# Kernel optimization log

Hardware: AMD Instinct MI355X
Metric: run time of the kernel (lower is better)

## Reference

```python
import jax, jax.numpy as jnp
import numpy as np
from functools import partial

K = 64
KERNEL_SIZE = 16
TAU = 10.0
THETA = 0.5
GAMMA = 10.0
ALPHA = float(np.exp(-1.0 / TAU))
BETA = 1.0 - ALPHA

@jax.custom_vjp
def spike(x):
    return (x >= 0).astype(x.dtype)

def _spike_fwd(x):
    return spike(x), x

def _spike_bwd(x, g):
    surrogate = GAMMA * jnp.maximum(1.0 - GAMMA * jnp.abs(x), 0.0)
    return (g * surrogate,)

spike.defvjp(_spike_fwd, _spike_bwd)

def setup_inputs() -> dict:
    key = jax.random.key(0)
    k1, k2 = jax.random.split(key)
    B, T = 256, 4096
    x = jax.random.normal(k1, (B, 1, T), dtype=jnp.float32)
    # conv weight [K, 1, ks], init N(0, 1/sqrt(ks))
    W = jax.random.normal(k2, (K, 1, KERNEL_SIZE), dtype=jnp.float32) / np.sqrt(KERNEL_SIZE)
    return {"x": x, "W": W}

def _forward(x, W):
    B = x.shape[0]
    x = x.reshape(B, 1, -1)  # [B,1,T]
    # causal conv: left pad ks-1 -> output length T
    u = jax.lax.conv_general_dilated(
        x, W,
        window_strides=(1,),
        padding=[(KERNEL_SIZE - 1, 0)],
        dimension_numbers=("NCH", "OIH", "NCH"),
    )  # [B,K,T]
    u_t = jnp.transpose(u, (2, 0, 1))  # [T,B,K]
    v0 = jnp.zeros((B, K), dtype=x.dtype)

    def step(v, ut):
        v = ALPHA * v + BETA * ut                      # leak + input
        s_raw = spike(v - THETA)                        # [B,K]
        winner = jax.lax.stop_gradient(jnp.argmax(v, axis=1))  # [B]
        winner_spiked = jnp.take_along_axis(s_raw, winner[:, None], axis=1)  # [B,1]
        wta_mask = jax.nn.one_hot(winner, K, dtype=s_raw.dtype) * winner_spiked
        s = s_raw * wta_mask
        v = v - s * THETA                               # reset
        return v, s

    _, spikes_t = jax.lax.scan(step, v0, u_t)  # [T,B,K]
    return jnp.transpose(spikes_t, (1, 2, 0))  # [B,K,T]

def reference(x, W):
    return _forward(x, W)
```

## Files before the change

kernel.cpp:

```cpp
#include <hip/hip_runtime.h>

#define T_LEN  4096
#define KS     16
#define NSEG   8
#define SEG_CH 32
#define WARM_CH 20
#define USTRIDE 18

#define ALPHA_F 0.9048374180359595f
#define BETA_F  0.09516258196404048f
#define THETA_F 0.5f

__device__ __forceinline__ float wave64_max_all(float v) {
  float m, t;
  asm("s_nop 1\n\t"
      "v_max_f32 %0, %2, %2 quad_perm:[1,0,3,2] row_mask:0xf bank_mask:0xf\n\t"
      "s_nop 1\n\t"
      "v_max_f32 %0, %0, %0 quad_perm:[2,3,0,1] row_mask:0xf bank_mask:0xf\n\t"
      "s_nop 1\n\t"
      "v_max_f32 %0, %0, %0 row_half_mirror row_mask:0xf bank_mask:0xf\n\t"
      "s_nop 1\n\t"
      "v_max_f32 %0, %0, %0 row_mirror row_mask:0xf bank_mask:0xf\n\t"
      "v_mov_b32 %1, %0\n\t"
      "s_nop 1\n\t"
      "v_permlane32_swap_b32 %1, %0\n\t"
      "s_nop 1\n\t"
      "v_max_f32 %0, %0, %1\n\t"
      "v_mov_b32 %1, %0\n\t"
      "s_nop 1\n\t"
      "v_permlane16_swap_b32 %1, %0\n\t"
      "s_nop 1\n\t"
      "v_max_f32 %0, %0, %1"
      : "=&v"(m), "=&v"(t)
      : "v"(v));
  return m;
}

__global__ __launch_bounds__(128, 4)
void convlif_wta_kernel(const float* __restrict__ x, const float* __restrict__ W,
                        float* __restrict__ out) {
  const int blk  = blockIdx.x;
  const int b    = blk >> 3;
  const int seg  = blk & (NSEG - 1);
  const int wave = threadIdx.x >> 6;
  const int lane = threadIdx.x & 63;

  const int cout0  = seg * SEG_CH;
  const int cstart = (cout0 > WARM_CH) ? (cout0 - WARM_CH) : 0;
  const int cend   = cout0 + SEG_CH;
  const int wpairs = (cout0 - cstart) >> 1;
  const int npair  = (cend - cstart) >> 1;

  __shared__ float dbuf[2][2][64][USTRIDE];

  const float4* xv4 = reinterpret_cast<const float4*>(x + (size_t)b * T_LEN);
  float* orow = out + ((size_t)(b * 64 + lane)) * T_LEN;

  if (wave == 1) {
    float w[KS];
    {
      const float4* w4 = reinterpret_cast<const float4*>(W + lane * KS);
      #pragma unroll
      for (int q = 0; q < 4; ++q) {
        float4 a = w4[q];
        w[4*q+0] = a.x; w[4*q+1] = a.y; w[4*q+2] = a.z; w[4*q+3] = a.w;
      }
    }

    for (int p = 0; p < npair; ++p) {
      #pragma unroll
      for (int ch = 0; ch < 2; ++ch) {
        const int c = cstart + 2 * p + ch;
        float xf[32];
        if (c == 0) {
          #pragma unroll
          for (int m = 0; m < 16; ++m) xf[m] = 0.0f;
        } else {
          const int b4 = 4 * c - 4;
          #pragma unroll
          for (int q = 0; q < 4; ++q) {
            float4 a = xv4[b4 + q];
            xf[4*q+0] = a.x; xf[4*q+1] = a.y; xf[4*q+2] = a.z; xf[4*q+3] = a.w;
          }
        }
        #pragma unroll
        for (int q = 0; q < 4; ++q) {
          float4 a = xv4[4*c + q];
          xf[16+4*q+0] = a.x; xf[16+4*q+1] = a.y;
          xf[16+4*q+2] = a.z; xf[16+4*q+3] = a.w;
        }

        float* ur = &dbuf[p & 1][ch][lane][0];
        #pragma unroll
        for (int i = 0; i < 16; i += 2) {
          float acc0 = w[0] * xf[1 + i];
          #pragma unroll
          for (int j = 1; j < KS; ++j) acc0 = fmaf(w[j], xf[1 + i + j], acc0);
          float acc1 = w[0] * xf[2 + i];
          #pragma unroll
          for (int j = 1; j < KS; ++j) acc1 = fmaf(w[j], xf[2 + i + j], acc1);
          *reinterpret_cast<float2*>(ur + i) =
              make_float2(BETA_F * acc0, BETA_F * acc1);
        }
      }
      __syncthreads();
    }
    __syncthreads();
  } else {
    float v = 0.0f;

    __syncthreads();

    for (int q = 0; q < wpairs; ++q) {
      const int slot = q & 1;
      #pragma unroll
      for (int ch = 0; ch < 2; ++ch) {
        float u[16];
        {
          const float* ur = &dbuf[slot][ch][lane][0];
          #pragma unroll
          for (int i = 0; i < 16; i += 2) {
            float2 t2 = *reinterpret_cast<const float2*>(ur + i);
            u[i] = t2.x; u[i + 1] = t2.y;
          }
        }
        #pragma unroll
        for (int i = 0; i < 16; ++i) {
          float vr = fmaf(ALPHA_F, v, u[i]);
          float vm = vr - THETA_F;
          unsigned long long sp = __ballot(vr >= THETA_F);
          bool c1 = (vr >= THETA_F);
          v = c1 ? vm : vr;
          if (__builtin_expect((sp & (sp - 1ull)) != 0ull, 0)) {
            float m = wave64_max_all(vr);
            unsigned long long eq = __ballot(vr == m);
            bool win = (lane == __builtin_ctzll(eq));
            v = win ? vm : vr;
          }
        }
      }
      __syncthreads();
    }

    for (int q = wpairs; q < npair; ++q) {
      const int slot = q & 1;
      #pragma unroll
      for (int ch = 0; ch < 2; ++ch) {
        const int c = cstart + 2 * q + ch;
        float u[16];
        {
          const float* ur = &dbuf[slot][ch][lane][0];
          #pragma unroll
          for (int i = 0; i < 16; i += 2) {
            float2 t2 = *reinterpret_cast<const float2*>(ur + i);
            u[i] = t2.x; u[i + 1] = t2.y;
          }
        }
        float sv[16];
        #pragma unroll
        for (int i = 0; i < 16; ++i) {
          float vr = fmaf(ALPHA_F, v, u[i]);
          float vm = vr - THETA_F;
          unsigned long long sp = __ballot(vr >= THETA_F);
          bool c1 = (vr >= THETA_F);
          sv[i] = c1 ? 1.0f : 0.0f;
          v     = c1 ? vm : vr;
          if (__builtin_expect((sp & (sp - 1ull)) != 0ull, 0)) {
            float m = wave64_max_all(vr);
            unsigned long long eq = __ballot(vr == m);
            bool win = (lane == __builtin_ctzll(eq));
            sv[i] = win ? 1.0f : 0.0f;
            v     = win ? vm : vr;
          }
        }
        float4* pp = reinterpret_cast<float4*>(orow + (size_t)c * 16);
        pp[0] = make_float4(sv[0],  sv[1],  sv[2],  sv[3]);
        pp[1] = make_float4(sv[4],  sv[5],  sv[6],  sv[7]);
        pp[2] = make_float4(sv[8],  sv[9],  sv[10], sv[11]);
        pp[3] = make_float4(sv[12], sv[13], sv[14], sv[15]);
      }
      __syncthreads();
    }
  }
}

extern "C" void kernel_launch(void* const* d_in, const int* in_sizes, int n_in,
                              void* d_out, int out_size, void* d_ws, size_t ws_size,
                              hipStream_t stream) {
  const float* x   = (const float*)d_in[0];
  const float* W   = (const float*)d_in[1];
  float*       out = (float*)d_out;
  convlif_wta_kernel<<<dim3(256 * NSEG), dim3(128), 0, stream>>>(x, W, out);
}
```

Baseline: 106.1 us.

## Use three conv producer waves and halve time segments per batch row

Time is now split into 4 segments of 64 chunks instead of 8 segments of 32. Each block gets three producer waves that compute the convolution for three chunks per barrier interval into a triple-wide double buffer, feeding one scan wave. Fewer segments cut the duplicated warm-up scan work. The extra producer waves are meant to stop the single conv wave from limiting the serial scan. The trade-off is a longer serial scan per block and half as many blocks, which lowers parallelism across the GPU.

Result: slower. 148.6 us (+40.1%).

```diff
diff --git a/kernel.cpp b/kernel.cpp
--- a/kernel.cpp
+++ b/kernel.cpp
@@ -2,8 +2,8 @@
 
 #define T_LEN  4096
 #define KS     16
-#define NSEG   8
-#define SEG_CH 32
+#define NSEG   4
+#define SEG_CH 64
 #define WARM_CH 20
 #define USTRIDE 18
 
@@ -36,11 +36,11 @@
   return m;
 }
 
-__global__ __launch_bounds__(128, 4)
+__global__ __launch_bounds__(256, 4)
 void convlif_wta_kernel(const float* __restrict__ x, const float* __restrict__ W,
                         float* __restrict__ out) {
   const int blk  = blockIdx.x;
-  const int b    = blk >> 3;
+  const int b    = blk >> 2;
   const int seg  = blk & (NSEG - 1);
   const int wave = threadIdx.x >> 6;
   const int lane = threadIdx.x & 63;
@@ -48,15 +48,16 @@
   const int cout0  = seg * SEG_CH;
   const int cstart = (cout0 > WARM_CH) ? (cout0 - WARM_CH) : 0;
   const int cend   = cout0 + SEG_CH;
-  const int wpairs = (cout0 - cstart) >> 1;
-  const int npair  = (cend - cstart) >> 1;
+  const int nch    = cend - cstart;
+  const int nIv    = (nch + 2) / 3;
 
-  __shared__ float dbuf[2][2][64][USTRIDE];
+  __shared__ float dbuf[2][3][64][USTRIDE];
 
   const float4* xv4 = reinterpret_cast<const float4*>(x + (size_t)b * T_LEN);
   float* orow = out + ((size_t)(b * 64 + lane)) * T_LEN;
 
-  if (wave == 1) {
+  if (wave >= 1) {
+    const int j = wave - 1;
     float w[KS];
     {
       const float4* w4 = reinterpret_cast<const float4*>(W + lane * KS);
@@ -67,117 +68,110 @@
       }
     }
 
-    for (int p = 0; p < npair; ++p) {
+    auto conv_into = [&](int c, int slot) {
+      float xf[32];
+      if (c == 0) {
+        #pragma unroll
+        for (int m = 0; m < 16; ++m) xf[m] = 0.0f;
+      } else {
+        const int b4 = 4 * c - 4;
+        #pragma unroll
+        for (int q = 0; q < 4; ++q) {
+          float4 a = xv4[b4 + q];
+          xf[4*q+0] = a.x; xf[4*q+1] = a.y; xf[4*q+2] = a.z; xf[4*q+3] = a.w;
+        }
+      }
       #pragma unroll
-      for (int ch = 0; ch < 2; ++ch) {
-        const int c = cstart + 2 * p + ch;
-        float xf[32];
-        if (c == 0) {
-          #pragma unroll
-          for (int m = 0; m < 16; ++m) xf[m] = 0.0f;
-        } else {
-          const int b4 = 4 * c - 4;
-          #pragma unroll
-          for (int q = 0; q < 4; ++q) {
-            float4 a = xv4[b4 + q];
-            xf[4*q+0] = a.x; xf[4*q+1] = a.y; xf[4*q+2] = a.z; xf[4*q+3] = a.w;
+      for (int q = 0; q < 4; ++q) {
+        float4 a = xv4[4*c + q];
+        xf[16+4*q+0] = a.x; xf[16+4*q+1] = a.y;
+        xf[16+4*q+2] = a.z; xf[16+4*q+3] = a.w;
+      }
+      float* ur = &dbuf[slot][j][lane][0];
+      #pragma unroll
+      for (int i = 0; i < 16; i += 2) {
+        float acc0 = w[0] * xf[1 + i];
+        #pragma unroll
+        for (int jj = 1; jj < KS; ++jj) acc0 = fmaf(w[jj], xf[1 + i + jj], acc0);
+        float acc1 = w[0] * xf[2 + i];
+        #pragma unroll
+        for (int jj = 1; jj < KS; ++jj) acc1 = fmaf(w[jj], xf[2 + i + jj], acc1);
+        *reinterpret_cast<float2*>(ur + i) =
+            make_float2(BETA_F * acc0, BETA_F * acc1);
+      }
+    };
+
+    {
+      const int cc = cstart + j;
+      if (cc < cend) conv_into(cc, 0);
+    }
+    __syncthreads();
+
+    for (int p = 0; p < nIv; ++p) {
+      const int cc = cstart + 3 * (p + 1) + j;
+      if (cc < cend) conv_into(cc, (p + 1) & 1);
+      __syncthreads();
+    }
+  } else {
+    float v = 0.0f;
+    __syncthreads();
+
+    for (int p = 0; p < nIv; ++p) {
+      const int slot = p & 1;
+      const int base = cstart + 3 * p;
+      #pragma unroll
+      for (int ch = 0; ch < 3; ++ch) {
+        const int c = base + ch;
+        if (c < cend) {
+          float u[16];
+          {
+            const float* ur = &dbuf[slot][ch][lane][0];
+            #pragma unroll
+            for (int i = 0; i < 16; i += 2) {
+              float2 t2 = *reinterpret_cast<const float2*>(ur + i);
+              u[i] = t2.x; u[i + 1] = t2.y;
+            }
+          }
+          if (c >= cout0) {
+            float sv[16];
+            #pragma unroll
+            for (int i = 0; i < 16; ++i) {
+              float vr = fmaf(ALPHA_F, v, u[i]);
+              float vm = vr - THETA_F;
+              unsigned long long sp = __ballot(vr >= THETA_F);
+              bool c1 = (vr >= THETA_F);
+              sv[i] = c1 ? 1.0f : 0.0f;
+              v     = c1 ? vm : vr;
+              if (__builtin_expect((sp & (sp - 1ull)) != 0ull, 0)) {
+                float m = wave64_max_all(vr);
+                unsigned long long eq = __ballot(vr == m);
+                bool win = (lane == __builtin_ctzll(eq));
+                sv[i] = win ? 1.0f : 0.0f;
+                v     = win ? vm : vr;
+              }
+            }
+            float4* pp = reinterpret_cast<float4*>(orow + (size_t)c * 16);
+            pp[0] = make_float4(sv[0],  sv[1],  sv[2],  sv[3]);
+            pp[1] = make_float4(sv[4],  sv[5],  sv[6],  sv[7]);
+            pp[2] = make_float4(sv[8],  sv[9],  sv[10], sv[11]);
+            pp[3] = make_float4(sv[12], sv[13], sv[14], sv[15]);
+          } else {
+            #pragma unroll
+            for (int i = 0; i < 16; ++i) {
+              float vr = fmaf(ALPHA_F, v, u[i]);
+              float vm = vr - THETA_F;
+              unsigned long long sp = __ballot(vr >= THETA_F);
+              bool c1 = (vr >= THETA_F);
+              v = c1 ? vm : vr;
+              if (__builtin_expect((sp & (sp - 1ull)) != 0ull, 0)) {
+                float m = wave64_max_all(vr);
+                unsigned long long eq = __ballot(vr == m);
+                bool win = (lane == __builtin_ctzll(eq));
+                v = win ? vm : vr;
+              }
+            }
           }
         }
-        #pragma unroll
-        for (int q = 0; q < 4; ++q) {
-          float4 a = xv4[4*c + q];
-          xf[16+4*q+0] = a.x; xf[16+4*q+1] = a.y;
-          xf[16+4*q+2] = a.z; xf[16+4*q+3] = a.w;
-        }
-
-        float* ur = &dbuf[p & 1][ch][lane][0];
-        #pragma unroll
-        for (int i = 0; i < 16; i += 2) {
-          float acc0 = w[0] * xf[1 + i];
-          #pragma unroll
-          for (int j = 1; j < KS; ++j) acc0 = fmaf(w[j], xf[1 + i + j], acc0);
-          float acc1 = w[0] * xf[2 + i];
-          #pragma unroll
-          for (int j = 1; j < KS; ++j) acc1 = fmaf(w[j], xf[2 + i + j], acc1);
-          *reinterpret_cast<float2*>(ur + i) =
-              make_float2(BETA_F * acc0, BETA_F * acc1);
-        }
-      }
-      __syncthreads();
-    }
-    __syncthreads();
-  } else {
-    float v = 0.0f;
-
-    __syncthreads();
-
-    for (int q = 0; q < wpairs; ++q) {
-      const int slot = q & 1;
-      #pragma unroll
-      for (int ch = 0; ch < 2; ++ch) {
-        float u[16];
-        {
-          const float* ur = &dbuf[slot][ch][lane][0];
-          #pragma unroll
-          for (int i = 0; i < 16; i += 2) {
-            float2 t2 = *reinterpret_cast<const float2*>(ur + i);
-            u[i] = t2.x; u[i + 1] = t2.y;
-          }
-        }
-        #pragma unroll
-        for (int i = 0; i < 16; ++i) {
-          float vr = fmaf(ALPHA_F, v, u[i]);
-          float vm = vr - THETA_F;
-          unsigned long long sp = __ballot(vr >= THETA_F);
-          bool c1 = (vr >= THETA_F);
-          v = c1 ? vm : vr;
-          if (__builtin_expect((sp & (sp - 1ull)) != 0ull, 0)) {
-            float m = wave64_max_all(vr);
-            unsigned long long eq = __ballot(vr == m);
-            bool win = (lane == __builtin_ctzll(eq));
-            v = win ? vm : vr;
-          }
-        }
-      }
-      __syncthreads();
-    }
-
-    for (int q = wpairs; q < npair; ++q) {
-      const int slot = q & 1;
-      #pragma unroll
-      for (int ch = 0; ch < 2; ++ch) {
-        const int c = cstart + 2 * q + ch;
-        float u[16];
-        {
-          const float* ur = &dbuf[slot][ch][lane][0];
-          #pragma unroll
-          for (int i = 0; i < 16; i += 2) {
-            float2 t2 = *reinterpret_cast<const float2*>(ur + i);
-            u[i] = t2.x; u[i + 1] = t2.y;
-          }
-        }
-        float sv[16];
-        #pragma unroll
-        for (int i = 0; i < 16; ++i) {
-          float vr = fmaf(ALPHA_F, v, u[i]);
-          float vm = vr - THETA_F;
-          unsigned long long sp = __ballot(vr >= THETA_F);
-          bool c1 = (vr >= THETA_F);
-          sv[i] = c1 ? 1.0f : 0.0f;
-          v     = c1 ? vm : vr;
-          if (__builtin_expect((sp & (sp - 1ull)) != 0ull, 0)) {
-            float m = wave64_max_all(vr);
-            unsigned long long eq = __ballot(vr == m);
-            bool win = (lane == __builtin_ctzll(eq));
-            sv[i] = win ? 1.0f : 0.0f;
-            v     = win ? vm : vr;
-          }
-        }
-        float4* pp = reinterpret_cast<float4*>(orow + (size_t)c * 16);
-        pp[0] = make_float4(sv[0],  sv[1],  sv[2],  sv[3]);
-        pp[1] = make_float4(sv[4],  sv[5],  sv[6],  sv[7]);
-        pp[2] = make_float4(sv[8],  sv[9],  sv[10], sv[11]);
-        pp[3] = make_float4(sv[12], sv[13], sv[14], sv[15]);
       }
       __syncthreads();
     }
@@ -190,5 +184,5 @@
   const float* x   = (const float*)d_in[0];
   const float* W   = (const float*)d_in[1];
   float*       out = (float*)d_out;
-  convlif_wta_kernel<<<dim3(256 * NSEG), dim3(128), 0, stream>>>(x, W, out);
+  convlif_wta_kernel<<<dim3(256 * NSEG), dim3(256), 0, stream>>>(x, W, out);
 }
```
